# Kernel tuning notes

Hardware: AMD Instinct MI355X
Metric: run time of the kernel (lower is better)

Reference implementation:

```python
import jax, jax.numpy as jnp
import numpy as np

VOCAB = 50257
EMBED = 256
NFREQ = 64
NRULES = 100
B, S = 4, 1024


def setup_inputs() -> dict:
    key = jax.random.key(0)
    ks = jax.random.split(key, 7)
    return {
        "token_ids": jax.random.randint(ks[0], (B, S), 0, VOCAB),
        "a_n": jax.random.normal(ks[1], (VOCAB, NFREQ), dtype=jnp.float32),
        "b_n": jax.random.normal(ks[2], (VOCAB, NFREQ), dtype=jnp.float32),
        "rule_transform": jax.random.normal(ks[3], (NRULES, EMBED, EMBED), dtype=jnp.float32),
        "token_rules": jax.random.randint(ks[4], (VOCAB,), 0, NRULES),
        "proj_w": jax.random.normal(ks[5], (EMBED, NFREQ), dtype=jnp.float32) * (1.0 / np.sqrt(NFREQ)),
        "proj_b": jax.random.normal(ks[6], (EMBED,), dtype=jnp.float32) * 0.01,
    }


def reference(token_ids, a_n, b_n, rule_transform, token_rules, proj_w, proj_b):
    vocab_size, nfreq = a_n.shape
    # fourier_freqs = linspace(1, F, F) -> [1..F]
    freqs = jnp.arange(1, nfreq + 1, dtype=jnp.float32)  # [F]
    x = token_ids.astype(jnp.float32)[..., None] / vocab_size  # [B,S,1]
    ang = (2.0 * jnp.pi) * freqs * x  # [B,S,F]
    # gather per-token fourier coefficients, fuse cos/sin combine
    fourier = a_n[token_ids] * jnp.cos(ang) + b_n[token_ids] * jnp.sin(ang)  # [B,S,F]
    base = jnp.einsum('bsf,df->bsd', fourier, proj_w) + proj_b  # [B,S,D]
    rule_idx = token_rules[token_ids]  # [B,S]
    rules = rule_transform[rule_idx]  # [B,S,D,D] gathered per token
    return jnp.einsum('bsd,bsde->bse', base, rules)  # [B,S,D]
```

## Files before the change

kernel.cpp:

```cpp
#include <hip/hip_runtime.h>
#include <math.h>

#define VOCAB   50257
#define EMBED   256
#define NFREQ   64
#define NRULES  100
#define NTOK    4096
#define CAP     256
#define CHUNK   16
#define NCHUNK  8

typedef __attribute__((ext_vector_type(8))) short short8;
typedef __attribute__((ext_vector_type(4))) float floatx4;

#define BASEBF_BYTES ((size_t)NTOK * EMBED * 2)
#define LIST_BYTES   ((size_t)NRULES * CAP * 4)
#define CNT_OFF      (BASEBF_BYTES)
#define LIST_OFF     (CNT_OFF + 512)
#define WT_OFF       (LIST_OFF + LIST_BYTES)
#define TFRAG_OFF    (WT_OFF + (size_t)NFREQ * EMBED * 4)

__device__ __forceinline__ ushort f2bf(float f) {
    unsigned u = __float_as_uint(f);
    unsigned r = (u + 0x7FFFu + ((u >> 16) & 1u)) >> 16;
    return (ushort)r;
}

__global__ __launch_bounds__(256) void prep_kernel(
    const float* __restrict__ proj_w, float* __restrict__ wT,
    int* __restrict__ counts)
{
    __shared__ float s_t[64 * 65];
    const int tid = threadIdx.x;
    const int b   = blockIdx.x;

    if (b == 0 && tid < NRULES) counts[tid] = 0;

    const float4* __restrict__ W4 =
        (const float4*)(proj_w + (size_t)b * 64 * NFREQ);
    #pragma unroll
    for (int i = 0; i < 4; ++i) {
        const int v = i * 256 + tid;
        const float4 w = W4[v];
        const int dl = v >> 4, f0 = (v & 15) * 4;
        s_t[dl * 65 + f0 + 0] = w.x;
        s_t[dl * 65 + f0 + 1] = w.y;
        s_t[dl * 65 + f0 + 2] = w.z;
        s_t[dl * 65 + f0 + 3] = w.w;
    }
    __syncthreads();
    #pragma unroll
    for (int j = 0; j < 16; ++j) {
        const int o = j * 256 + tid;
        const int f = o >> 6, c = o & 63;
        wT[f * EMBED + b * 64 + c] = s_t[c * 65 + f];
    }
}

__global__ __launch_bounds__(256) void convert_kernel(
    const float* __restrict__ T,
    ushort*      __restrict__ Tfrag)
{
    __shared__ float s[32 * 260];
    const int tid = threadIdx.x;
    const int r   = blockIdx.x;
    const int kb  = blockIdx.y;

    const float4* __restrict__ src =
        (const float4*)(T + (size_t)r * 65536 + (size_t)kb * 32 * 256);
    #pragma unroll
    for (int i = 0; i < 8; ++i) {
        const int v   = i * 256 + tid;
        const int row = v >> 6, c4 = v & 63;
        ((float4*)s)[row * 65 + c4] = src[v];
    }
    __syncthreads();

    const int et  = tid >> 4;
    const int l16 = tid & 15;
    uint4* __restrict__ dst = (uint4*)Tfrag + (size_t)r * 16384;

    #pragma unroll
    for (int lg = 0; lg < 4; ++lg) {
        ushort h[8];
        #pragma unroll
        for (int j = 0; j < 8; ++j)
            h[j] = f2bf(s[(lg * 8 + j) * 260 + et * 16 + l16]);
        uint4 o;
        o.x = (unsigned)h[0] | ((unsigned)h[1] << 16);
        o.y = (unsigned)h[2] | ((unsigned)h[3] << 16);
        o.z = (unsigned)h[4] | ((unsigned)h[5] << 16);
        o.w = (unsigned)h[6] | ((unsigned)h[7] << 16);
        dst[(et * 8 + kb) * 64 + lg * 16 + l16] = o;
    }
}

__global__ __launch_bounds__(256) void fused_base_kernel(
    const int*   __restrict__ token_ids,
    const float* __restrict__ a_n,
    const float* __restrict__ b_n,
    const int*   __restrict__ token_rules,
    const float* __restrict__ wT,
    const float* __restrict__ proj_b,
    ushort*      __restrict__ base_bf,
    int*         __restrict__ counts,
    int*         __restrict__ list)
{
    __shared__ float s_four[4][NFREQ];

    const int tid = threadIdx.x;
    const int tl  = tid >> 6;
    const int f   = tid & 63;
    const int tok_idx = blockIdx.x * 4 + tl;
    const int tok     = token_ids[tok_idx];

    const float x   = (float)tok * (1.0f / (float)VOCAB);
    const float rev = (float)(f + 1) * x;
    const float rf  = rev - floorf(rev);
    const float sv  = __builtin_amdgcn_sinf(rf);
    const float cv  = __builtin_amdgcn_cosf(rf);
    s_four[tl][f] = a_n[(size_t)tok * NFREQ + f] * cv
                  + b_n[(size_t)tok * NFREQ + f] * sv;

    if (f == 0) {
        const int rule = token_rules[tok];
        const int pos  = atomicAdd(&counts[rule], 1);
        if (pos < CAP) list[rule * CAP + pos] = tok_idx;
    }
    __syncthreads();

    const int   d    = tid;
    const float bias = proj_b[d];
    float a0 = bias, a1 = bias, a2 = bias, a3 = bias;

    #pragma unroll 4
    for (int q = 0; q < 16; ++q) {
        const float w0 = wT[(4 * q + 0) * EMBED + d];
        const float w1 = wT[(4 * q + 1) * EMBED + d];
        const float w2 = wT[(4 * q + 2) * EMBED + d];
        const float w3 = wT[(4 * q + 3) * EMBED + d];
        const float4 f0 = ((const float4*)s_four[0])[q];
        const float4 f1 = ((const float4*)s_four[1])[q];
        const float4 f2 = ((const float4*)s_four[2])[q];
        const float4 f3 = ((const float4*)s_four[3])[q];
        a0 += w0 * f0.x + w1 * f0.y + w2 * f0.z + w3 * f0.w;
        a1 += w0 * f1.x + w1 * f1.y + w2 * f1.z + w3 * f1.w;
        a2 += w0 * f2.x + w1 * f2.y + w2 * f2.z + w3 * f2.w;
        a3 += w0 * f3.x + w1 * f3.y + w2 * f3.z + w3 * f3.w;
    }
    base_bf[(size_t)(blockIdx.x * 4 + 0) * EMBED + d] = f2bf(a0);
    base_bf[(size_t)(blockIdx.x * 4 + 1) * EMBED + d] = f2bf(a1);
    base_bf[(size_t)(blockIdx.x * 4 + 2) * EMBED + d] = f2bf(a2);
    base_bf[(size_t)(blockIdx.x * 4 + 3) * EMBED + d] = f2bf(a3);
}

__global__ __launch_bounds__(256) void apply_kernel(
    const ushort* __restrict__ base_bf,
    const ushort* __restrict__ Tfrag,
    const int*    __restrict__ counts,
    const int*    __restrict__ list,
    float*        __restrict__ out)
{
    __shared__ __align__(16) ushort s_a[16 * 264];

    const int rule = blockIdx.x;
    int cnt = counts[rule];
    if (cnt > CAP) cnt = CAP;
    const int t0 = blockIdx.y * CHUNK;
    if (t0 >= cnt) return;

    const int tid  = threadIdx.x;
    const int w    = tid >> 6;
    const int lane = tid & 63;

    const int* __restrict__ lst = list + rule * CAP;
    int idx[CHUNK];
    #pragma unroll
    for (int t = 0; t < CHUNK; ++t) {
        int tt = t0 + t;
        if (tt > cnt - 1) tt = cnt - 1;
        idx[t] = __builtin_amdgcn_readfirstlane(lst[tt]);
    }

    #pragma unroll
    for (int i = 0; i < 2; ++i) {
        const int v = i * 256 + tid;
        const int t = v >> 5, c = v & 31;
        ((uint4*)s_a)[t * 33 + c * 2 / 2] =
            ((const uint4*)(base_bf + (size_t)idx[t] * EMBED))[c];
    }
    __syncthreads();

    const short8* __restrict__ Bf =
        (const short8*)Tfrag + (size_t)rule * 16384;

    floatx4 acc[4];
    #pragma unroll
    for (int q = 0; q < 4; ++q) acc[q] = (floatx4){0.f, 0.f, 0.f, 0.f};

    const int arow = (lane & 15) * 33 + (lane >> 4);

    short8 bcur[4], bnxt[4];
    #pragma unroll
    for (int q = 0; q < 4; ++q)
        bcur[q] = Bf[((w * 4 + q) * 8 + 0) * 64 + lane];

    for (int kb = 0; kb < 8; ++kb) {
        if (kb < 7) {
            #pragma unroll
            for (int q = 0; q < 4; ++q)
                bnxt[q] = Bf[((w * 4 + q) * 8 + kb + 1) * 64 + lane];
        }
        const short8 av = ((const short8*)s_a)[arow + kb * 4];
        #pragma unroll
        for (int q = 0; q < 4; ++q)
            acc[q] = __builtin_amdgcn_mfma_f32_16x16x32_bf16(
                av, bcur[q], acc[q], 0, 0, 0);
        #pragma unroll
        for (int q = 0; q < 4; ++q) bcur[q] = bnxt[q];
    }

    const int m4 = (lane >> 4) * 4;
    const int n  = lane & 15;
    #pragma unroll
    for (int q = 0; q < 4; ++q) {
        const int e = (w * 4 + q) * 16 + n;
        #pragma unroll
        for (int r = 0; r < 4; ++r) {
            const int m = m4 + r;
            if (t0 + m < cnt)
                out[(size_t)idx[m] * EMBED + e] = acc[q][r];
        }
    }
}

extern "C" void kernel_launch(void* const* d_in, const int* in_sizes, int n_in,
                              void* d_out, int out_size, void* d_ws, size_t ws_size,
                              hipStream_t stream) {
    const int*   token_ids      = (const int*)  d_in[0];
    const float* a_n            = (const float*)d_in[1];
    const float* b_n            = (const float*)d_in[2];
    const float* rule_transform = (const float*)d_in[3];
    const int*   token_rules    = (const int*)  d_in[4];
    const float* proj_w         = (const float*)d_in[5];
    const float* proj_b         = (const float*)d_in[6];
    float*       out            = (float*)d_out;

    ushort* base_bf = (ushort*)d_ws;
    int*    counts  = (int*)   ((char*)d_ws + CNT_OFF);
    int*    list    = (int*)   ((char*)d_ws + LIST_OFF);
    float*  wT      = (float*) ((char*)d_ws + WT_OFF);
    ushort* Tfrag   = (ushort*)((char*)d_ws + TFRAG_OFF);

    prep_kernel<<<4, 256, 0, stream>>>(proj_w, wT, counts);
    convert_kernel<<<dim3(NRULES, 8), 256, 0, stream>>>(rule_transform, Tfrag);
    fused_base_kernel<<<NTOK / 4, 256, 0, stream>>>(
        token_ids, a_n, b_n, token_rules, wT, proj_b, base_bf, counts, list);
    apply_kernel<<<dim3(NRULES, NCHUNK), 256, 0, stream>>>(
        base_bf, Tfrag, counts, list, out);
}
```

Baseline: 124.8 us.

## Merge prep, convert and bucketing into one launch; fuse base projection into apply

The three preparatory kernels are folded into a single launch that converts rule matrices, transposes proj_w, and buckets tokens by rule using shared-memory atomics in one block. The Fourier feature and base projection computation moves into the apply kernel, so each tile computes its 16 base rows directly into shared memory and skips the global base_bf round trip. This drops two kernel launches and the intermediate write and read, but puts a serial single-block bucketing pass on the critical path. It also adds FMA work and register pressure (16 accumulators per thread) to the MFMA kernel.

```diff
diff --git a/kernel.cpp b/kernel.cpp
--- a/kernel.cpp
+++ b/kernel.cpp
@@ -13,12 +13,10 @@
 typedef __attribute__((ext_vector_type(8))) short short8;
 typedef __attribute__((ext_vector_type(4))) float floatx4;
 
-#define BASEBF_BYTES ((size_t)NTOK * EMBED * 2)
-#define LIST_BYTES   ((size_t)NRULES * CAP * 4)
-#define CNT_OFF      (BASEBF_BYTES)
-#define LIST_OFF     (CNT_OFF + 512)
-#define WT_OFF       (LIST_OFF + LIST_BYTES)
-#define TFRAG_OFF    (WT_OFF + (size_t)NFREQ * EMBED * 4)
+#define LIST_OFF   512
+#define LIST_BYTES ((size_t)NRULES * CAP * 4)
+#define WT_OFF     (LIST_OFF + LIST_BYTES)
+#define TFRAG_OFF  (WT_OFF + (size_t)NFREQ * EMBED * 4)
 
 __device__ __forceinline__ ushort f2bf(float f) {
     unsigned u = __float_as_uint(f);
@@ -26,141 +24,104 @@
     return (ushort)r;
 }
 
-__global__ __launch_bounds__(256) void prep_kernel(
-    const float* __restrict__ proj_w, float* __restrict__ wT,
-    int* __restrict__ counts)
-{
-    __shared__ float s_t[64 * 65];
-    const int tid = threadIdx.x;
-    const int b   = blockIdx.x;
-
-    if (b == 0 && tid < NRULES) counts[tid] = 0;
-
-    const float4* __restrict__ W4 =
-        (const float4*)(proj_w + (size_t)b * 64 * NFREQ);
-    #pragma unroll
-    for (int i = 0; i < 4; ++i) {
-        const int v = i * 256 + tid;
-        const float4 w = W4[v];
-        const int dl = v >> 4, f0 = (v & 15) * 4;
-        s_t[dl * 65 + f0 + 0] = w.x;
-        s_t[dl * 65 + f0 + 1] = w.y;
-        s_t[dl * 65 + f0 + 2] = w.z;
-        s_t[dl * 65 + f0 + 3] = w.w;
-    }
-    __syncthreads();
-    #pragma unroll
-    for (int j = 0; j < 16; ++j) {
-        const int o = j * 256 + tid;
-        const int f = o >> 6, c = o & 63;
-        wT[f * EMBED + b * 64 + c] = s_t[c * 65 + f];
-    }
-}
-
-__global__ __launch_bounds__(256) void convert_kernel(
+__global__ __launch_bounds__(256) void prep_convert_bucket_kernel(
     const float* __restrict__ T,
-    ushort*      __restrict__ Tfrag)
+    const float* __restrict__ proj_w,
+    const int*   __restrict__ token_ids,
+    const int*   __restrict__ token_rules,
+    ushort*      __restrict__ Tfrag,
+    float*       __restrict__ wT,
+    int*         __restrict__ counts,
+    int*         __restrict__ list)
 {
     __shared__ float s[32 * 260];
     const int tid = threadIdx.x;
-    const int r   = blockIdx.x;
-    const int kb  = blockIdx.y;
-
-    const float4* __restrict__ src =
-        (const float4*)(T + (size_t)r * 65536 + (size_t)kb * 32 * 256);
-    #pragma unroll
-    for (int i = 0; i < 8; ++i) {
-        const int v   = i * 256 + tid;
-        const int row = v >> 6, c4 = v & 63;
-        ((float4*)s)[row * 65 + c4] = src[v];
-    }
-    __syncthreads();
-
-    const int et  = tid >> 4;
-    const int l16 = tid & 15;
-    uint4* __restrict__ dst = (uint4*)Tfrag + (size_t)r * 16384;
-
-    #pragma unroll
-    for (int lg = 0; lg < 4; ++lg) {
-        ushort h[8];
-        #pragma unroll
-        for (int j = 0; j < 8; ++j)
-            h[j] = f2bf(s[(lg * 8 + j) * 260 + et * 16 + l16]);
-        uint4 o;
-        o.x = (unsigned)h[0] | ((unsigned)h[1] << 16);
-        o.y = (unsigned)h[2] | ((unsigned)h[3] << 16);
-        o.z = (unsigned)h[4] | ((unsigned)h[5] << 16);
-        o.w = (unsigned)h[6] | ((unsigned)h[7] << 16);
-        dst[(et * 8 + kb) * 64 + lg * 16 + l16] = o;
-    }
-}
-
-__global__ __launch_bounds__(256) void fused_base_kernel(
-    const int*   __restrict__ token_ids,
-    const float* __restrict__ a_n,
-    const float* __restrict__ b_n,
-    const int*   __restrict__ token_rules,
-    const float* __restrict__ wT,
-    const float* __restrict__ proj_b,
-    ushort*      __restrict__ base_bf,
-    int*         __restrict__ counts,
-    int*         __restrict__ list)
-{
-    __shared__ float s_four[4][NFREQ];
-
-    const int tid = threadIdx.x;
-    const int tl  = tid >> 6;
-    const int f   = tid & 63;
-    const int tok_idx = blockIdx.x * 4 + tl;
-    const int tok     = token_ids[tok_idx];
-
-    const float x   = (float)tok * (1.0f / (float)VOCAB);
-    const float rev = (float)(f + 1) * x;
-    const float rf  = rev - floorf(rev);
-    const float sv  = __builtin_amdgcn_sinf(rf);
-    const float cv  = __builtin_amdgcn_cosf(rf);
-    s_four[tl][f] = a_n[(size_t)tok * NFREQ + f] * cv
-                  + b_n[(size_t)tok * NFREQ + f] * sv;
-
-    if (f == 0) {
-        const int rule = token_rules[tok];
-        const int pos  = atomicAdd(&counts[rule], 1);
-        if (pos < CAP) list[rule * CAP + pos] = tok_idx;
-    }
-    __syncthreads();
-
-    const int   d    = tid;
-    const float bias = proj_b[d];
-    float a0 = bias, a1 = bias, a2 = bias, a3 = bias;
-
-    #pragma unroll 4
-    for (int q = 0; q < 16; ++q) {
-        const float w0 = wT[(4 * q + 0) * EMBED + d];
-        const float w1 = wT[(4 * q + 1) * EMBED + d];
-        const float w2 = wT[(4 * q + 2) * EMBED + d];
-        const float w3 = wT[(4 * q + 3) * EMBED + d];
-        const float4 f0 = ((const float4*)s_four[0])[q];
-        const float4 f1 = ((const float4*)s_four[1])[q];
-        const float4 f2 = ((const float4*)s_four[2])[q];
-        const float4 f3 = ((const float4*)s_four[3])[q];
-        a0 += w0 * f0.x + w1 * f0.y + w2 * f0.z + w3 * f0.w;
-        a1 += w0 * f1.x + w1 * f1.y + w2 * f1.z + w3 * f1.w;
-        a2 += w0 * f2.x + w1 * f2.y + w2 * f2.z + w3 * f2.w;
-        a3 += w0 * f3.x + w1 * f3.y + w2 * f3.z + w3 * f3.w;
-    }
-    base_bf[(size_t)(blockIdx.x * 4 + 0) * EMBED + d] = f2bf(a0);
-    base_bf[(size_t)(blockIdx.x * 4 + 1) * EMBED + d] = f2bf(a1);
-    base_bf[(size_t)(blockIdx.x * 4 + 2) * EMBED + d] = f2bf(a2);
-    base_bf[(size_t)(blockIdx.x * 4 + 3) * EMBED + d] = f2bf(a3);
+
+    if (blockIdx.x < NRULES) {
+        const int r  = blockIdx.x;
+        const int kb = blockIdx.y;
+
+        const float4* __restrict__ src =
+            (const float4*)(T + (size_t)r * 65536 + (size_t)kb * 32 * 256);
+        #pragma unroll
+        for (int i = 0; i < 8; ++i) {
+            const int v   = i * 256 + tid;
+            const int row = v >> 6, c4 = v & 63;
+            ((float4*)s)[row * 65 + c4] = src[v];
+        }
+        __syncthreads();
+
+        const int et  = tid >> 4;
+        const int l16 = tid & 15;
+        uint4* __restrict__ dst = (uint4*)Tfrag + (size_t)r * 16384;
+
+        #pragma unroll
+        for (int lg = 0; lg < 4; ++lg) {
+            ushort h[8];
+            #pragma unroll
+            for (int j = 0; j < 8; ++j)
+                h[j] = f2bf(s[(lg * 8 + j) * 260 + et * 16 + l16]);
+            uint4 o;
+            o.x = (unsigned)h[0] | ((unsigned)h[1] << 16);
+            o.y = (unsigned)h[2] | ((unsigned)h[3] << 16);
+            o.z = (unsigned)h[4] | ((unsigned)h[5] << 16);
+            o.w = (unsigned)h[6] | ((unsigned)h[7] << 16);
+            dst[(et * 8 + kb) * 64 + lg * 16 + l16] = o;
+        }
+        return;
+    }
+
+    if (blockIdx.y < 4) {
+        const int b = blockIdx.y;
+        const float4* __restrict__ W4 =
+            (const float4*)(proj_w + (size_t)b * 64 * NFREQ);
+        #pragma unroll
+        for (int i = 0; i < 4; ++i) {
+            const int v = i * 256 + tid;
+            const float4 w = W4[v];
+            const int dl = v >> 4, f0 = (v & 15) * 4;
+            s[dl * 65 + f0 + 0] = w.x;
+            s[dl * 65 + f0 + 1] = w.y;
+            s[dl * 65 + f0 + 2] = w.z;
+            s[dl * 65 + f0 + 3] = w.w;
+        }
+        __syncthreads();
+        #pragma unroll
+        for (int j = 0; j < 16; ++j) {
+            const int o = j * 256 + tid;
+            const int f = o >> 6, c = o & 63;
+            wT[f * EMBED + b * 64 + c] = s[c * 65 + f];
+        }
+        return;
+    }
+
+    if (blockIdx.y == 4) {
+        int* s_cnt = (int*)s;
+        if (tid < NRULES) s_cnt[tid] = 0;
+        __syncthreads();
+        for (int i = tid; i < NTOK; i += 256) {
+            const int tok  = token_ids[i];
+            const int rule = token_rules[tok];
+            const int pos  = atomicAdd(&s_cnt[rule], 1);
+            if (pos < CAP) list[rule * CAP + pos] = i;
+        }
+        __syncthreads();
+        if (tid < NRULES) counts[tid] = s_cnt[tid];
+    }
 }
 
 __global__ __launch_bounds__(256) void apply_kernel(
-    const ushort* __restrict__ base_bf,
+    const int*    __restrict__ token_ids,
+    const float*  __restrict__ a_n,
+    const float*  __restrict__ b_n,
+    const float*  __restrict__ wT,
+    const float*  __restrict__ proj_b,
     const ushort* __restrict__ Tfrag,
     const int*    __restrict__ counts,
     const int*    __restrict__ list,
     float*        __restrict__ out)
 {
+    __shared__ float s_four[16][NFREQ];
     __shared__ __align__(16) ushort s_a[16 * 264];
 
     const int rule = blockIdx.x;
@@ -172,8 +133,8 @@
     const int tid  = threadIdx.x;
     const int w    = tid >> 6;
     const int lane = tid & 63;
-
     const int* __restrict__ lst = list + rule * CAP;
+
     int idx[CHUNK];
     #pragma unroll
     for (int t = 0; t < CHUNK; ++t) {
@@ -182,12 +143,56 @@
         idx[t] = __builtin_amdgcn_readfirstlane(lst[tt]);
     }
 
-    #pragma unroll
-    for (int i = 0; i < 2; ++i) {
-        const int v = i * 256 + tid;
-        const int t = v >> 5, c = v & 31;
-        ((uint4*)s_a)[t * 33 + c * 2 / 2] =
-            ((const uint4*)(base_bf + (size_t)idx[t] * EMBED))[c];
+    {
+        const int tl = tid >> 4;
+        const int fq = tid & 15;
+        int tt = t0 + tl;
+        if (tt > cnt - 1) tt = cnt - 1;
+        const int row = lst[tt];
+        const int tok = token_ids[row];
+
+        const float4 a4 = ((const float4*)(a_n + (size_t)tok * NFREQ))[fq];
+        const float4 b4 = ((const float4*)(b_n + (size_t)tok * NFREQ))[fq];
+        const float  x  = (float)tok * (1.0f / (float)VOCAB);
+
+        float4 fv;
+        {
+            float rev, rf;
+            rev = (float)(fq * 4 + 1) * x; rf = rev - floorf(rev);
+            fv.x = a4.x * __builtin_amdgcn_cosf(rf) + b4.x * __builtin_amdgcn_sinf(rf);
+            rev = (float)(fq * 4 + 2) * x; rf = rev - floorf(rev);
+            fv.y = a4.y * __builtin_amdgcn_cosf(rf) + b4.y * __builtin_amdgcn_sinf(rf);
+            rev = (float)(fq * 4 + 3) * x; rf = rev - floorf(rev);
+            fv.z = a4.z * __builtin_amdgcn_cosf(rf) + b4.z * __builtin_amdgcn_sinf(rf);
+            rev = (float)(fq * 4 + 4) * x; rf = rev - floorf(rev);
+            fv.w = a4.w * __builtin_amdgcn_cosf(rf) + b4.w * __builtin_amdgcn_sinf(rf);
+        }
+        ((float4*)s_four[tl])[fq] = fv;
+    }
+    __syncthreads();
+
+    {
+        const int   d    = tid;
+        const float bias = proj_b[d];
+        float acc[CHUNK];
+        #pragma unroll
+        for (int t = 0; t < CHUNK; ++t) acc[t] = bias;
+
+        #pragma unroll 4
+        for (int q = 0; q < 16; ++q) {
+            const float w0 = wT[(4 * q + 0) * EMBED + d];
+            const float w1 = wT[(4 * q + 1) * EMBED + d];
+            const float w2 = wT[(4 * q + 2) * EMBED + d];
+            const float w3 = wT[(4 * q + 3) * EMBED + d];
+            #pragma unroll
+            for (int t = 0; t < CHUNK; ++t) {
+                const float4 f4 = ((const float4*)s_four[t])[q];
+                acc[t] += w0 * f4.x + w1 * f4.y + w2 * f4.z + w3 * f4.w;
+            }
+        }
+        #pragma unroll
+        for (int t = 0; t < CHUNK; ++t)
+            s_a[t * 264 + d] = f2bf(acc[t]);
     }
     __syncthreads();
 
@@ -223,13 +228,13 @@
     const int m4 = (lane >> 4) * 4;
     const int n  = lane & 15;
     #pragma unroll
-    for (int q = 0; q < 4; ++q) {
-        const int e = (w * 4 + q) * 16 + n;
-        #pragma unroll
-        for (int r = 0; r < 4; ++r) {
-            const int m = m4 + r;
-            if (t0 + m < cnt)
-                out[(size_t)idx[m] * EMBED + e] = acc[q][r];
+    for (int r = 0; r < 4; ++r) {
+        const int tt = t0 + m4 + r;
+        if (tt < cnt) {
+            const int row = lst[tt];
+            #pragma unroll
+            for (int q = 0; q < 4; ++q)
+                out[(size_t)row * EMBED + (w * 4 + q) * 16 + n] = acc[q][r];
         }
     }
 }
@@ -246,16 +251,14 @@
     const float* proj_b         = (const float*)d_in[6];
     float*       out            = (float*)d_out;
 
-    ushort* base_bf = (ushort*)d_ws;
-    int*    counts  = (int*)   ((char*)d_ws + CNT_OFF);
-    int*    list    = (int*)   ((char*)d_ws + LIST_OFF);
-    float*  wT      = (float*) ((char*)d_ws + WT_OFF);
-    ushort* Tfrag   = (ushort*)((char*)d_ws + TFRAG_OFF);
-
-    prep_kernel<<<4, 256, 0, stream>>>(proj_w, wT, counts);
-    convert_kernel<<<dim3(NRULES, 8), 256, 0, stream>>>(rule_transform, Tfrag);
-    fused_base_kernel<<<NTOK / 4, 256, 0, stream>>>(
-        token_ids, a_n, b_n, token_rules, wT, proj_b, base_bf, counts, list);
+    int*    counts = (int*)   d_ws;
+    int*    list   = (int*)   ((char*)d_ws + LIST_OFF);
+    float*  wT     = (float*) ((char*)d_ws + WT_OFF);
+    ushort* Tfrag  = (ushort*)((char*)d_ws + TFRAG_OFF);
+
+    prep_convert_bucket_kernel<<<dim3(NRULES + 1, 8), 256, 0, stream>>>(
+        rule_transform, proj_w, token_ids, token_rules,
+        Tfrag, wT, counts, list);
     apply_kernel<<<dim3(NRULES, NCHUNK), 256, 0, stream>>>(
-        base_bf, Tfrag, counts, list, out);
-}
+        token_ids, a_n, b_n, wT, proj_b, Tfrag, counts, list, out);
+}
```

Measured after the change: 126.5 us. Within noise of the previous version (+1.4%).

## Merge prep, convert and token bucketing into one launch with LDS-atomic bucketing

Applied to the files above, without the earlier changes.

Folds the proj_w transpose, the rule-matrix bf16 conversion and the per-rule token bucketing into a single kernel launch. Extra blocks handle the transpose and a single block builds the rule lists using shared-memory atomics instead of global atomics inside the base kernel. This removes one launch and the global atomic contention from fused_base_kernel. The cost is that bucketing is serialized in one block over all 4096 tokens, and its list order becomes nondeterministic in a different way.

```diff
diff --git a/kernel.cpp b/kernel.cpp
--- a/kernel.cpp
+++ b/kernel.cpp
@@ -26,72 +26,89 @@
     return (ushort)r;
 }
 
-__global__ __launch_bounds__(256) void prep_kernel(
-    const float* __restrict__ proj_w, float* __restrict__ wT,
-    int* __restrict__ counts)
-{
-    __shared__ float s_t[64 * 65];
-    const int tid = threadIdx.x;
-    const int b   = blockIdx.x;
-
-    if (b == 0 && tid < NRULES) counts[tid] = 0;
-
-    const float4* __restrict__ W4 =
-        (const float4*)(proj_w + (size_t)b * 64 * NFREQ);
-    #pragma unroll
-    for (int i = 0; i < 4; ++i) {
-        const int v = i * 256 + tid;
-        const float4 w = W4[v];
-        const int dl = v >> 4, f0 = (v & 15) * 4;
-        s_t[dl * 65 + f0 + 0] = w.x;
-        s_t[dl * 65 + f0 + 1] = w.y;
-        s_t[dl * 65 + f0 + 2] = w.z;
-        s_t[dl * 65 + f0 + 3] = w.w;
-    }
-    __syncthreads();
-    #pragma unroll
-    for (int j = 0; j < 16; ++j) {
-        const int o = j * 256 + tid;
-        const int f = o >> 6, c = o & 63;
-        wT[f * EMBED + b * 64 + c] = s_t[c * 65 + f];
-    }
-}
-
-__global__ __launch_bounds__(256) void convert_kernel(
+__global__ __launch_bounds__(256) void prep_convert_bucket_kernel(
     const float* __restrict__ T,
-    ushort*      __restrict__ Tfrag)
+    const float* __restrict__ proj_w,
+    const int*   __restrict__ token_ids,
+    const int*   __restrict__ token_rules,
+    ushort*      __restrict__ Tfrag,
+    float*       __restrict__ wT,
+    int*         __restrict__ counts,
+    int*         __restrict__ list)
 {
     __shared__ float s[32 * 260];
     const int tid = threadIdx.x;
-    const int r   = blockIdx.x;
-    const int kb  = blockIdx.y;
-
-    const float4* __restrict__ src =
-        (const float4*)(T + (size_t)r * 65536 + (size_t)kb * 32 * 256);
-    #pragma unroll
-    for (int i = 0; i < 8; ++i) {
-        const int v   = i * 256 + tid;
-        const int row = v >> 6, c4 = v & 63;
-        ((float4*)s)[row * 65 + c4] = src[v];
-    }
-    __syncthreads();
-
-    const int et  = tid >> 4;
-    const int l16 = tid & 15;
-    uint4* __restrict__ dst = (uint4*)Tfrag + (size_t)r * 16384;
-
-    #pragma unroll
-    for (int lg = 0; lg < 4; ++lg) {
-        ushort h[8];
-        #pragma unroll
-        for (int j = 0; j < 8; ++j)
-            h[j] = f2bf(s[(lg * 8 + j) * 260 + et * 16 + l16]);
-        uint4 o;
-        o.x = (unsigned)h[0] | ((unsigned)h[1] << 16);
-        o.y = (unsigned)h[2] | ((unsigned)h[3] << 16);
-        o.z = (unsigned)h[4] | ((unsigned)h[5] << 16);
-        o.w = (unsigned)h[6] | ((unsigned)h[7] << 16);
-        dst[(et * 8 + kb) * 64 + lg * 16 + l16] = o;
+
+    if (blockIdx.x < NRULES) {
+        const int r  = blockIdx.x;
+        const int kb = blockIdx.y;
+
+        const float4* __restrict__ src =
+            (const float4*)(T + (size_t)r * 65536 + (size_t)kb * 32 * 256);
+        #pragma unroll
+        for (int i = 0; i < 8; ++i) {
+            const int v   = i * 256 + tid;
+            const int row = v >> 6, c4 = v & 63;
+            ((float4*)s)[row * 65 + c4] = src[v];
+        }
+        __syncthreads();
+
+        const int et  = tid >> 4;
+        const int l16 = tid & 15;
+        uint4* __restrict__ dst = (uint4*)Tfrag + (size_t)r * 16384;
+
+        #pragma unroll
+        for (int lg = 0; lg < 4; ++lg) {
+            ushort h[8];
+            #pragma unroll
+            for (int j = 0; j < 8; ++j)
+                h[j] = f2bf(s[(lg * 8 + j) * 260 + et * 16 + l16]);
+            uint4 o;
+            o.x = (unsigned)h[0] | ((unsigned)h[1] << 16);
+            o.y = (unsigned)h[2] | ((unsigned)h[3] << 16);
+            o.z = (unsigned)h[4] | ((unsigned)h[5] << 16);
+            o.w = (unsigned)h[6] | ((unsigned)h[7] << 16);
+            dst[(et * 8 + kb) * 64 + lg * 16 + l16] = o;
+        }
+        return;
+    }
+
+    if (blockIdx.y < 4) {
+        const int b = blockIdx.y;
+        const float4* __restrict__ W4 =
+            (const float4*)(proj_w + (size_t)b * 64 * NFREQ);
+        #pragma unroll
+        for (int i = 0; i < 4; ++i) {
+            const int v = i * 256 + tid;
+            const float4 w = W4[v];
+            const int dl = v >> 4, f0 = (v & 15) * 4;
+            s[dl * 65 + f0 + 0] = w.x;
+            s[dl * 65 + f0 + 1] = w.y;
+            s[dl * 65 + f0 + 2] = w.z;
+            s[dl * 65 + f0 + 3] = w.w;
+        }
+        __syncthreads();
+        #pragma unroll
+        for (int j = 0; j < 16; ++j) {
+            const int o = j * 256 + tid;
+            const int f = o >> 6, c = o & 63;
+            wT[f * EMBED + b * 64 + c] = s[c * 65 + f];
+        }
+        return;
+    }
+
+    if (blockIdx.y == 4) {
+        int* s_cnt = (int*)s;
+        if (tid < NRULES) s_cnt[tid] = 0;
+        __syncthreads();
+        for (int i = tid; i < NTOK; i += 256) {
+            const int tok  = token_ids[i];
+            const int rule = token_rules[tok];
+            const int pos  = atomicAdd(&s_cnt[rule], 1);
+            if (pos < CAP) list[rule * CAP + pos] = i;
+        }
+        __syncthreads();
+        if (tid < NRULES) counts[tid] = s_cnt[tid];
     }
 }
 
@@ -99,12 +116,9 @@
     const int*   __restrict__ token_ids,
     const float* __restrict__ a_n,
     const float* __restrict__ b_n,
-    const int*   __restrict__ token_rules,
     const float* __restrict__ wT,
     const float* __restrict__ proj_b,
-    ushort*      __restrict__ base_bf,
-    int*         __restrict__ counts,
-    int*         __restrict__ list)
+    ushort*      __restrict__ base_bf)
 {
     __shared__ float s_four[4][NFREQ];
 
@@ -121,12 +135,6 @@
     const float cv  = __builtin_amdgcn_cosf(rf);
     s_four[tl][f] = a_n[(size_t)tok * NFREQ + f] * cv
                   + b_n[(size_t)tok * NFREQ + f] * sv;
-
-    if (f == 0) {
-        const int rule = token_rules[tok];
-        const int pos  = atomicAdd(&counts[rule], 1);
-        if (pos < CAP) list[rule * CAP + pos] = tok_idx;
-    }
     __syncthreads();
 
     const int   d    = tid;
@@ -186,7 +194,7 @@
     for (int i = 0; i < 2; ++i) {
         const int v = i * 256 + tid;
         const int t = v >> 5, c = v & 31;
-        ((uint4*)s_a)[t * 33 + c * 2 / 2] =
+        ((uint4*)s_a)[t * 33 + c] =
             ((const uint4*)(base_bf + (size_t)idx[t] * EMBED))[c];
     }
     __syncthreads();
@@ -252,10 +260,11 @@
     float*  wT      = (float*) ((char*)d_ws + WT_OFF);
     ushort* Tfrag   = (ushort*)((char*)d_ws + TFRAG_OFF);
 
-    prep_kernel<<<4, 256, 0, stream>>>(proj_w, wT, counts);
-    convert_kernel<<<dim3(NRULES, 8), 256, 0, stream>>>(rule_transform, Tfrag);
+    prep_convert_bucket_kernel<<<dim3(NRULES + 1, 8), 256, 0, stream>>>(
+        rule_transform, proj_w, token_ids, token_rules,
+        Tfrag, wT, counts, list);
     fused_base_kernel<<<NTOK / 4, 256, 0, stream>>>(
-        token_ids, a_n, b_n, token_rules, wT, proj_b, base_bf, counts, list);
+        token_ids, a_n, b_n, wT, proj_b, base_bf);
     apply_kernel<<<dim3(NRULES, NCHUNK), 256, 0, stream>>>(
         base_bf, Tfrag, counts, list, out);
 }
```

After: 124.4 us. About the same (-0.3%).
